# Kernel tuning notes

Measured on AMD Instinct MI355X. Metric: run time of the kernel, lower is better.

## Reference

```python
import jax, jax.numpy as jnp
import numpy as np

# Constants matching init_kwargs
N_HEADS = 8
D_MODEL = 256
PATCH_NUM = 128
D_K = D_MODEL // N_HEADS  # 32
TEMP = 0.5
EPS = 1e-10


def setup_inputs() -> dict:
    key = jax.random.key(0)
    ks = jax.random.split(key, 20)
    s = 0.02
    d, h, n = D_MODEL, N_HEADS, PATCH_NUM
    inp = {
        "x": jax.random.normal(ks[0], (32, n, d), dtype=jnp.float32),
        "gumbel_u": jax.random.uniform(ks[1], (h, n, n, 2), dtype=jnp.float32),
        "memory_w": jax.random.normal(ks[2], (n, h * d), dtype=jnp.float32) * s,
        "fc_out_w": jax.random.normal(ks[3], (2 * d, d), dtype=jnp.float32) * s,
        "fc_out_b": jnp.zeros((d,), jnp.float32),
        "fc_cat_w": jax.random.normal(ks[4], (d, 2), dtype=jnp.float32) * s,
        "fc_cat_b": jnp.zeros((2,), jnp.float32),
        "wq": jax.random.normal(ks[5], (d, d), dtype=jnp.float32) * s,
        "bq": jnp.zeros((d,), jnp.float32),
        "wk": jax.random.normal(ks[6], (d, d), dtype=jnp.float32) * s,
        "bk": jnp.zeros((d,), jnp.float32),
        "wv": jax.random.normal(ks[7], (d, d), dtype=jnp.float32) * s,
        "bv": jnp.zeros((d,), jnp.float32),
        "out_w": jax.random.normal(ks[8], (d, d), dtype=jnp.float32) * s,
        "out_b": jnp.zeros((d,), jnp.float32),
        "mlp_w1": jax.random.normal(ks[9], (d, d), dtype=jnp.float32) * s,
        "mlp_b1": jnp.zeros((d,), jnp.float32),
        "mlp_w2": jax.random.normal(ks[10], (d, d), dtype=jnp.float32) * s,
        "mlp_b2": jnp.zeros((d,), jnp.float32),
    }
    return inp


def _forward(x, memory_w, fc_out_w, fc_out_b, fc_cat_w, fc_cat_b,
             wq, bq, wk, bk, wv, bv, out_w, out_b,
             mlp_w1, mlp_b1, mlp_w2, mlp_b2, gumbel_u):
    H, N, D = N_HEADS, PATCH_NUM, D_MODEL
    B = x.shape[0]

    # ---- SSConnectionLearning on memory feats ----
    # memory: Embedding(N, d_model*n_heads) -> feats [H, N, D]
    feats = memory_w.reshape(N, H, D).transpose(1, 0, 2)
    # rel_rec gathers row index i (receiver), rel_send gathers col index j (sender)
    senders = jnp.broadcast_to(feats[:, None, :, :], (H, N, N, D))   # feats[j]
    receivers = jnp.broadcast_to(feats[:, :, None, :], (H, N, N, D))  # feats[i]
    pair = jnp.concatenate([senders, receivers], axis=-1)  # [H,N,N,2D]
    hdn = jax.nn.relu(jnp.einsum('hijc,cd->hijd', pair, fc_out_w) + fc_out_b)
    logits = jnp.einsum('hijd,dk->hijk', hdn, fc_cat_w) + fc_cat_b  # [H,N,N,2]

    # gumbel-softmax, hard=True, straight-through
    g = -jnp.log(-jnp.log(gumbel_u + EPS) + EPS)
    y_soft = jax.nn.softmax((logits + g) / TEMP, axis=-1)
    y_hard = jax.nn.one_hot(jnp.argmax(y_soft, axis=-1), 2, dtype=y_soft.dtype)
    y = jax.lax.stop_gradient(y_hard - y_soft) + y_soft
    conn = y[..., 1]  # [H,N,N] learned sparse connection mask

    # ---- PatchIntegration (GELU MLP, dropout = identity in eval) ----
    xm = jax.nn.gelu(x @ mlp_w1 + mlp_b1)
    xm = xm @ mlp_w2 + mlp_b2

    # ---- Multihead attention masked by connection matrix ----
    q = (xm @ wq + bq).reshape(B, N, H, D_K).transpose(0, 2, 1, 3)  # [B,H,N,dk]
    k = (xm @ wk + bk).reshape(B, N, H, D_K).transpose(0, 2, 1, 3)
    v = (xm @ wv + bv).reshape(B, N, H, D_K).transpose(0, 2, 1, 3)
    scale = D_K ** -0.5
    scores = jnp.einsum('bhqd,bhkd->bhqk', q, k) * scale
    # additive mask: blocked where conn==0 (large negative keeps softmax finite)
    scores = scores + (conn[None] - 1.0) * 1e9
    attn = jax.nn.softmax(scores, axis=-1)
    out = jnp.einsum('bhqk,bhkd->bhqd', attn, v)
    out = out.transpose(0, 2, 1, 3).reshape(B, N, H * D_K)
    out = out @ out_w + out_b
    return out


def reference(x, gumbel_u, memory_w, fc_out_w, fc_out_b, fc_cat_w, fc_cat_b,
              wq, bq, wk, bk, wv, bv, out_w, out_b,
              mlp_w1, mlp_b1, mlp_w2, mlp_b2):
    return _forward(x, memory_w, fc_out_w, fc_out_b, fc_cat_w, fc_cat_b,
                    wq, bq, wk, bk, wv, bv, out_w, out_b,
                    mlp_w1, mlp_b1, mlp_w2, mlp_b2, gumbel_u)
```

## Files before the change

kernel.cpp:

```cpp
#include <hip/hip_runtime.h>
#include <hip/hip_bf16.h>
#include <math.h>


typedef short short8 __attribute__((ext_vector_type(8)));
typedef float f32x4 __attribute__((ext_vector_type(4)));

union V8 { uint4 u; short8 s; };

__device__ __forceinline__ float gelu_f(float x) {
    float inner = 0.7978845608028654f * (x + 0.044715f * x * x * x);
    return 0.5f * x * (1.0f + tanhf(inner));
}
__device__ __forceinline__ void split_bf16(float x, ushort& h, ushort& l) {
    __hip_bfloat16 bh = __float2bfloat16(x);
    float hf = __bfloat162float(bh);
    __hip_bfloat16 bl = __float2bfloat16(x - hf);
    h = __builtin_bit_cast(ushort, bh);
    l = __builtin_bit_cast(ushort, bl);
}
__device__ __forceinline__ ushort bf16bits(float x) {
    return __builtin_bit_cast(ushort, __float2bfloat16(x));
}
__device__ __forceinline__ float bits_to_f(ushort v) {
    return __builtin_bit_cast(float, ((uint)v) << 16);
}
__device__ __forceinline__ short8 lds_frag(const ushort* p) {
    V8 v; v.u = *(const uint4*)p; return v.s;
}


__global__ __launch_bounds__(512) void k_wprep(
    const float* __restrict__ mlp_w1, const float* __restrict__ mlp_w2,
    const float* __restrict__ wq, const float* __restrict__ wk,
    const float* __restrict__ wv, const float* __restrict__ out_w,
    const float* __restrict__ fc_out_w,
    ushort* __restrict__ hi, ushort* __restrict__ lo) {
    __shared__ __align__(16) float xs2[2][32 * 132];
    int bx = blockIdx.x, t = threadIdx.x;
    int half = t >> 8, tl = t & 255;
    int job = bx * 2 + half;
    int m = job >> 4, ks = (job >> 1) & 7, nh = job & 1;
    const float* W = m == 0 ? mlp_w1 : m == 1 ? mlp_w2 : m == 2 ? wq :
                     m == 3 ? wk : m == 4 ? wv : m == 5 ? out_w :
                     m == 6 ? fc_out_w : fc_out_w + 65536;
    ushort* Hm = hi + m * 65536;
    ushort* Lm = lo + m * 65536;
    float* xs = xs2[half];
    #pragma unroll
    for (int p = 0; p < 4; ++p) {
        int idx = p * 256 + tl;
        int row = idx >> 5, c4 = (idx & 31) * 4;
        *(float4*)(xs + row * 132 + c4) =
            *(const float4*)(W + (ks * 32 + row) * 256 + nh * 128 + c4);
    }
    __syncthreads();
    int lane = tl & 63, lr = lane & 15, quad = lane >> 4;
    #pragma unroll
    for (int it = 0; it < 2; ++it) {
        int tgl = (tl >> 6) + 4 * it;
        int tg = nh * 8 + tgl;
        int nl = tgl * 16 + lr;
        ushort hb[8], lb[8];
        #pragma unroll
        for (int j = 0; j < 8; ++j)
            split_bf16(xs[(quad * 8 + j) * 132 + nl], hb[j], lb[j]);
        uint4 ph = { (uint)hb[0] | ((uint)hb[1] << 16), (uint)hb[2] | ((uint)hb[3] << 16),
                     (uint)hb[4] | ((uint)hb[5] << 16), (uint)hb[6] | ((uint)hb[7] << 16) };
        uint4 pl = { (uint)lb[0] | ((uint)lb[1] << 16), (uint)lb[2] | ((uint)lb[3] << 16),
                     (uint)lb[4] | ((uint)lb[5] << 16), (uint)lb[6] | ((uint)lb[7] << 16) };
        int idx = ((tg * 8 + ks) * 64 + lane) * 8;
        *(uint4*)(Hm + idx) = ph;
        *(uint4*)(Lm + idx) = pl;
    }
}

__global__ __launch_bounds__(512) void k_p2(
    const float* __restrict__ memory_w, const float* __restrict__ X,
    const ushort* __restrict__ Whi, const ushort* __restrict__ Wlo,
    const float* __restrict__ b1, const float* __restrict__ b2,
    const float* __restrict__ Bq, const float* __restrict__ Bk,
    const float* __restrict__ Bv,
    float* __restrict__ A, float* __restrict__ Bm,
    ushort* __restrict__ Q, ushort* __restrict__ K, ushort* __restrict__ V) {
    __shared__ __align__(16) union {
        struct { ushort xhi[16 * 264], xlo[16 * 264]; } f;
        struct {
            ushort aHi[16 * 264], aLo[16 * 264];
            ushort bHi[16 * 264], bLo[16 * 264];
        } g;
    } sm;
    int bx = blockIdx.x, t = threadIdx.x;
    if (bx < 64) {
        int rt = bx;
        #pragma unroll
        for (int ii = 0; ii < 2; ++ii) {
            int f4 = ii * 512 + t;
            int rr = f4 >> 6, c = (f4 & 63) * 4;
            int r = rt * 16 + rr;
            int h = r >> 7, n = r & 127;
            float4 xv = *(const float4*)(memory_w + n * 2048 + h * 256 + c);
            ushort hh[4], ll[4];
            split_bf16(xv.x, hh[0], ll[0]); split_bf16(xv.y, hh[1], ll[1]);
            split_bf16(xv.z, hh[2], ll[2]); split_bf16(xv.w, hh[3], ll[3]);
            uint2 ph = { (uint)hh[0] | ((uint)hh[1] << 16), (uint)hh[2] | ((uint)hh[3] << 16) };
            uint2 pl = { (uint)ll[0] | ((uint)ll[1] << 16), (uint)ll[2] | ((uint)ll[3] << 16) };
            *(uint2*)(sm.f.xhi + rr * 264 + c) = ph;
            *(uint2*)(sm.f.xlo + rr * 264 + c) = pl;
        }
        __syncthreads();
        int lane = t & 63, w = t >> 6;
        int lr = lane & 15, quad = lane >> 4;
        int msel = w & 1, cq = w >> 1;
        const uint4* H4 = (const uint4*)(Whi + (6 + msel) * 65536);
        const uint4* L4 = (const uint4*)(Wlo + (6 + msel) * 65536);
        const ushort* ah = sm.f.xhi + lr * 264 + quad * 8;
        const ushort* al = sm.f.xlo + lr * 264 + quad * 8;
        float* O = msel ? Bm : A;
        #pragma unroll
        for (int i = 0; i < 4; ++i) {
            int tg = cq * 4 + i;
            f32x4 acc = {};
            #pragma unroll
            for (int ks = 0; ks < 8; ++ks) {
                short8 a_h = lds_frag(ah + ks * 32);
                short8 a_l = lds_frag(al + ks * 32);
                int off = (tg * 8 + ks) * 64 + lane;
                V8 bh, bl; bh.u = H4[off]; bl.u = L4[off];
                acc = __builtin_amdgcn_mfma_f32_16x16x32_bf16(a_h, bh.s, acc, 0, 0, 0);
                acc = __builtin_amdgcn_mfma_f32_16x16x32_bf16(a_l, bh.s, acc, 0, 0, 0);
                acc = __builtin_amdgcn_mfma_f32_16x16x32_bf16(a_h, bl.s, acc, 0, 0, 0);
            }
            int n0 = tg * 16 + lr;
            #pragma unroll
            for (int r = 0; r < 4; ++r)
                O[(rt * 16 + quad * 4 + r) * 256 + n0] = acc[r];
        }
        return;
    }
    int r0 = (bx - 64) * 16;
    #pragma unroll
    for (int ii = 0; ii < 2; ++ii) {
        int f4 = ii * 512 + t;
        int row = f4 >> 6, c = (f4 & 63) * 4;
        float4 xv = *(const float4*)(X + (r0 + row) * 256 + c);
        ushort h[4], l[4];
        split_bf16(xv.x, h[0], l[0]); split_bf16(xv.y, h[1], l[1]);
        split_bf16(xv.z, h[2], l[2]); split_bf16(xv.w, h[3], l[3]);
        uint2 ph = { (uint)h[0] | ((uint)h[1] << 16), (uint)h[2] | ((uint)h[3] << 16) };
        uint2 pl = { (uint)l[0] | ((uint)l[1] << 16), (uint)l[2] | ((uint)l[3] << 16) };
        *(uint2*)(sm.g.aHi + row * 264 + c) = ph;
        *(uint2*)(sm.g.aLo + row * 264 + c) = pl;
    }
    __syncthreads();
    int lane = t & 63, w = t >> 6;
    int lr = lane & 15, quad = lane >> 4;
    int aoff = lr * 264 + quad * 8;
    {
        const uint4* H4 = (const uint4*)(Whi + 0 * 65536);
        const uint4* L4 = (const uint4*)(Wlo + 0 * 65536);
        f32x4 acc[2] = {};
        #pragma unroll
        for (int ks = 0; ks < 8; ++ks) {
            short8 a_h = lds_frag(sm.g.aHi + aoff + ks * 32);
            short8 a_l = lds_frag(sm.g.aLo + aoff + ks * 32);
            #pragma unroll
            for (int ti = 0; ti < 2; ++ti) {
                int off = ((w * 2 + ti) * 8 + ks) * 64 + lane;
                V8 bh, bl; bh.u = H4[off]; bl.u = L4[off];
                acc[ti] = __builtin_amdgcn_mfma_f32_16x16x32_bf16(a_h, bh.s, acc[ti], 0, 0, 0);
                acc[ti] = __builtin_amdgcn_mfma_f32_16x16x32_bf16(a_l, bh.s, acc[ti], 0, 0, 0);
                acc[ti] = __builtin_amdgcn_mfma_f32_16x16x32_bf16(a_h, bl.s, acc[ti], 0, 0, 0);
            }
        }
        #pragma unroll
        for (int ti = 0; ti < 2; ++ti) {
            int n0 = (w * 2 + ti) * 16 + lr;
            float bb = b1[n0];
            #pragma unroll
            for (int r = 0; r < 4; ++r) {
                float o = gelu_f(acc[ti][r] + bb);
                ushort hh, ll; split_bf16(o, hh, ll);
                int ad = (quad * 4 + r) * 264 + n0;
                sm.g.bHi[ad] = hh; sm.g.bLo[ad] = ll;
            }
        }
    }
    __syncthreads();
    {
        const uint4* H4 = (const uint4*)(Whi + 1 * 65536);
        const uint4* L4 = (const uint4*)(Wlo + 1 * 65536);
        f32x4 acc[2] = {};
        #pragma unroll
        for (int ks = 0; ks < 8; ++ks) {
            short8 a_h = lds_frag(sm.g.bHi + aoff + ks * 32);
            short8 a_l = lds_frag(sm.g.bLo + aoff + ks * 32);
            #pragma unroll
            for (int ti = 0; ti < 2; ++ti) {
                int off = ((w * 2 + ti) * 8 + ks) * 64 + lane;
                V8 bh, bl; bh.u = H4[off]; bl.u = L4[off];
                acc[ti] = __builtin_amdgcn_mfma_f32_16x16x32_bf16(a_h, bh.s, acc[ti], 0, 0, 0);
                acc[ti] = __builtin_amdgcn_mfma_f32_16x16x32_bf16(a_l, bh.s, acc[ti], 0, 0, 0);
                acc[ti] = __builtin_amdgcn_mfma_f32_16x16x32_bf16(a_h, bl.s, acc[ti], 0, 0, 0);
            }
        }
        __syncthreads();
        #pragma unroll
        for (int ti = 0; ti < 2; ++ti) {
            int n0 = (w * 2 + ti) * 16 + lr;
            float bb = b2[n0];
            #pragma unroll
            for (int r = 0; r < 4; ++r) {
                float o = acc[ti][r] + bb;
                ushort hh, ll; split_bf16(o, hh, ll);
                int ad = (quad * 4 + r) * 264 + n0;
                sm.g.aHi[ad] = hh; sm.g.aLo[ad] = ll;
            }
        }
    }
    __syncthreads();
    {
        const uint4* Hq = (const uint4*)(Whi + 2 * 65536);
        const uint4* Lq = (const uint4*)(Wlo + 2 * 65536);
        const uint4* Hk = (const uint4*)(Whi + 3 * 65536);
        const uint4* Lk = (const uint4*)(Wlo + 3 * 65536);
        const uint4* Hv = (const uint4*)(Whi + 4 * 65536);
        const uint4* Lv = (const uint4*)(Wlo + 4 * 65536);
        f32x4 aq[2] = {}, ak[2] = {}, av[2] = {};
        #pragma unroll 2
        for (int ks = 0; ks < 8; ++ks) {
            short8 a_h = lds_frag(sm.g.aHi + aoff + ks * 32);
            short8 a_l = lds_frag(sm.g.aLo + aoff + ks * 32);
            #pragma unroll
            for (int ti = 0; ti < 2; ++ti) {
                int off = ((w * 2 + ti) * 8 + ks) * 64 + lane;
                V8 qh, ql, kh, kl, vh, vl;
                qh.u = Hq[off]; ql.u = Lq[off];
                kh.u = Hk[off]; kl.u = Lk[off];
                vh.u = Hv[off]; vl.u = Lv[off];
                aq[ti] = __builtin_amdgcn_mfma_f32_16x16x32_bf16(a_h, qh.s, aq[ti], 0, 0, 0);
                aq[ti] = __builtin_amdgcn_mfma_f32_16x16x32_bf16(a_l, qh.s, aq[ti], 0, 0, 0);
                aq[ti] = __builtin_amdgcn_mfma_f32_16x16x32_bf16(a_h, ql.s, aq[ti], 0, 0, 0);
                ak[ti] = __builtin_amdgcn_mfma_f32_16x16x32_bf16(a_h, kh.s, ak[ti], 0, 0, 0);
                ak[ti] = __builtin_amdgcn_mfma_f32_16x16x32_bf16(a_l, kh.s, ak[ti], 0, 0, 0);
                ak[ti] = __builtin_amdgcn_mfma_f32_16x16x32_bf16(a_h, kl.s, ak[ti], 0, 0, 0);
                av[ti] = __builtin_amdgcn_mfma_f32_16x16x32_bf16(a_h, vh.s, av[ti], 0, 0, 0);
                av[ti] = __builtin_amdgcn_mfma_f32_16x16x32_bf16(a_l, vh.s, av[ti], 0, 0, 0);
                av[ti] = __builtin_amdgcn_mfma_f32_16x16x32_bf16(a_h, vl.s, av[ti], 0, 0, 0);
            }
        }
        #pragma unroll
        for (int ti = 0; ti < 2; ++ti) {
            int n0 = (w * 2 + ti) * 16 + lr;
            float bq = Bq[n0], bk = Bk[n0], bv = Bv[n0];
            #pragma unroll
            for (int r = 0; r < 4; ++r) {
                int go = (r0 + quad * 4 + r) * 256 + n0;
                Q[go] = bf16bits(aq[ti][r] + bq);
                K[go] = bf16bits(ak[ti][r] + bk);
                V[go] = bf16bits(av[ti][r] + bv);
            }
        }
    }
}

__global__ __launch_bounds__(512) void k_conn(
    const float* __restrict__ A, const float* __restrict__ Bmat,
    const float* __restrict__ fc_out_b, const float* __restrict__ fc_cat_w,
    const float* __restrict__ fc_cat_b, const float* __restrict__ gumbel_u,
    ushort* __restrict__ maskb) {
    __shared__ __align__(16) float sA[16 * 260], sB[32 * 260];
    int bx = blockIdx.x, t = threadIdx.x;
    int h = bx >> 5;
    int rem = bx & 31;
    int it = rem >> 3, jt = rem & 7;
    int i0 = it * 32, j0 = jt * 16;
    int jl = t & 15, il = t >> 4;
    #pragma unroll
    for (int p = 0; p < 6; ++p) {
        int id2 = p * 512 + t;
        if (id2 < 1024) {
            int rr = id2 >> 6, c = (id2 & 63) * 4;
            *(float4*)(sA + rr * 260 + c) =
                *(const float4*)(A + (h * 128 + j0 + rr) * 256 + c);
        } else {
            int id3 = id2 - 1024;
            int rr = id3 >> 6, c = (id3 & 63) * 4;
            float4 bv = *(const float4*)(Bmat + (h * 128 + i0 + rr) * 256 + c);
            float4 fb = *(const float4*)(fc_out_b + c);
            bv.x += fb.x; bv.y += fb.y; bv.z += fb.z; bv.w += fb.w;
            *(float4*)(sB + rr * 260 + c) = bv;
        }
    }
    __syncthreads();
    const float* Ar = sA + jl * 260;
    const float* Br = sB + il * 260;
    float l0 = fc_cat_b[0], l1 = fc_cat_b[1];
    #pragma unroll 4
    for (int d4 = 0; d4 < 64; ++d4) {
        int d = d4 * 4;
        float4 av = *(const float4*)(Ar + d);
        float4 bv = *(const float4*)(Br + d);
        float4 cwA = *(const float4*)(fc_cat_w + d * 2);
        float4 cwB = *(const float4*)(fc_cat_w + d * 2 + 4);
        float h0 = fmaxf(av.x + bv.x, 0.f);
        float h1 = fmaxf(av.y + bv.y, 0.f);
        float h2 = fmaxf(av.z + bv.z, 0.f);
        float h3 = fmaxf(av.w + bv.w, 0.f);
        l0 += h0 * cwA.x + h1 * cwA.z + h2 * cwB.x + h3 * cwB.z;
        l1 += h0 * cwA.y + h1 * cwA.w + h2 * cwB.y + h3 * cwB.w;
    }
    int i = i0 + il, j = j0 + jl;
    float2 uu = *(const float2*)(gumbel_u + ((h * 128 + i) * 128 + j) * 2);
    float g0 = -logf(-logf(uu.x + 1e-10f) + 1e-10f);
    float g1 = -logf(-logf(uu.y + 1e-10f) + 1e-10f);
    bool on = (l1 + g1) > (l0 + g0);
    maskb[(h * 128 + i) * 128 + j] = bf16bits(on ? 0.f : -1e9f);
}

__global__ __launch_bounds__(256) void k_attn_mfma(
    const ushort* __restrict__ Q, const ushort* __restrict__ K,
    const ushort* __restrict__ V, const ushort* __restrict__ maskb,
    float* __restrict__ AO) {
    int bx = blockIdx.x;
    int b = bx >> 4, h = (bx >> 1) & 7, rh = bx & 1;
    int t = threadIdx.x;
    int lane = t & 63, w = t >> 6;
    __shared__ __align__(16) ushort vT[32 * 136];
    __shared__ __align__(16) ushort ps[64 * 136];
    #pragma unroll
    for (int it = 0; it < 2; ++it) {
        int idx = it * 256 + t;
        int key = idx >> 2, dq8 = (idx & 3) * 8;
        V8 vv; vv.u = *(const uint4*)(V + (b * 128 + key) * 256 + h * 32 + dq8);
        #pragma unroll
        for (int m = 0; m < 8; ++m)
            vT[(dq8 + m) * 136 + key] = (ushort)vv.s[m];
    }
    __syncthreads();
    int lr = lane & 15, quad = lane >> 4;
    int rt = rh * 4 + w;
    V8 af;
    af.u = *(const uint4*)(Q + (b * 128 + rt * 16 + lr) * 256 + h * 32 + quad * 8);
    f32x4 s[8];
    #pragma unroll
    for (int ct = 0; ct < 8; ++ct) {
        V8 bf_;
        bf_.u = *(const uint4*)(K + (b * 128 + ct * 16 + lr) * 256 + h * 32 + quad * 8);
        f32x4 z = {0.f, 0.f, 0.f, 0.f};
        s[ct] = __builtin_amdgcn_mfma_f32_16x16x32_bf16(af.s, bf_.s, z, 0, 0, 0);
    }
    const float scale = 0.17677669529663687f;
    const ushort* mrow = maskb + h * 16384;
    #pragma unroll
    for (int r = 0; r < 4; ++r) {
        int lrow = w * 16 + quad * 4 + r;
        int grow = rt * 16 + quad * 4 + r;
        float sv[8];
        float mx = -3.0e38f;
        #pragma unroll
        for (int ct = 0; ct < 8; ++ct) {
            float bias = bits_to_f(mrow[grow * 128 + ct * 16 + lr]);
            sv[ct] = s[ct][r] * scale + bias;
            mx = fmaxf(mx, sv[ct]);
        }
        mx = fmaxf(mx, __shfl_xor(mx, 1));
        mx = fmaxf(mx, __shfl_xor(mx, 2));
        mx = fmaxf(mx, __shfl_xor(mx, 4));
        mx = fmaxf(mx, __shfl_xor(mx, 8));
        float sum = 0.f;
        #pragma unroll
        for (int ct = 0; ct < 8; ++ct) {
            sv[ct] = __expf(sv[ct] - mx);
            sum += sv[ct];
        }
        sum += __shfl_xor(sum, 1);
        sum += __shfl_xor(sum, 2);
        sum += __shfl_xor(sum, 4);
        sum += __shfl_xor(sum, 8);
        float iv = 1.f / sum;
        #pragma unroll
        for (int ct = 0; ct < 8; ++ct)
            ps[lrow * 136 + ct * 16 + lr] = bf16bits(sv[ct] * iv);
    }
    f32x4 o0 = {}, o1 = {};
    #pragma unroll
    for (int kk = 0; kk < 4; ++kk) {
        short8 pa = lds_frag(ps + (w * 16 + lr) * 136 + kk * 32 + quad * 8);
        short8 v0 = lds_frag(vT + lr * 136 + kk * 32 + quad * 8);
        short8 v1 = lds_frag(vT + (16 + lr) * 136 + kk * 32 + quad * 8);
        o0 = __builtin_amdgcn_mfma_f32_16x16x32_bf16(pa, v0, o0, 0, 0, 0);
        o1 = __builtin_amdgcn_mfma_f32_16x16x32_bf16(pa, v1, o1, 0, 0, 0);
    }
    #pragma unroll
    for (int r = 0; r < 4; ++r) {
        int grow = rt * 16 + quad * 4 + r;
        float* op = AO + b * 32768 + grow * 256 + h * 32;
        op[lr] = o0[r];
        op[16 + lr] = o1[r];
    }
}

__global__ __launch_bounds__(256) void k_gemm16(
    const float* __restrict__ X, const ushort* __restrict__ Whi,
    const ushort* __restrict__ Wlo, const float* __restrict__ bias,
    float* __restrict__ Y) {
    __shared__ __align__(16) ushort xhi[16 * 264], xlo[16 * 264];
    int t = threadIdx.x;
    int r0 = blockIdx.x * 16;
    #pragma unroll
    for (int ii = 0; ii < 4; ++ii) {
        int f4 = ii * 256 + t;
        int row = f4 >> 6, c = (f4 & 63) * 4;
        float4 xv = *(const float4*)(X + (r0 + row) * 256 + c);
        ushort h[4], l[4];
        split_bf16(xv.x, h[0], l[0]); split_bf16(xv.y, h[1], l[1]);
        split_bf16(xv.z, h[2], l[2]); split_bf16(xv.w, h[3], l[3]);
        uint2 ph = { (uint)h[0] | ((uint)h[1] << 16), (uint)h[2] | ((uint)h[3] << 16) };
        uint2 pl = { (uint)l[0] | ((uint)l[1] << 16), (uint)l[2] | ((uint)l[3] << 16) };
        *(uint2*)(xhi + row * 264 + c) = ph;
        *(uint2*)(xlo + row * 264 + c) = pl;
    }
    __syncthreads();
    int l = t & 63, w = t >> 6;
    int lr = l & 15, quad = l >> 4;
    int tg = blockIdx.y * 4 + w;
    const ushort* ah = xhi + lr * 264 + quad * 8;
    const ushort* al = xlo + lr * 264 + quad * 8;
    const uint4* H4 = (const uint4*)Whi;
    const uint4* L4 = (const uint4*)Wlo;
    f32x4 acc = {};
    #pragma unroll
    for (int ks = 0; ks < 8; ++ks) {
        short8 a_h = lds_frag(ah + ks * 32);
        short8 a_l = lds_frag(al + ks * 32);
        int off = (tg * 8 + ks) * 64 + l;
        V8 bh, bl; bh.u = H4[off]; bl.u = L4[off];
        acc = __builtin_amdgcn_mfma_f32_16x16x32_bf16(a_h, bh.s, acc, 0, 0, 0);
        acc = __builtin_amdgcn_mfma_f32_16x16x32_bf16(a_l, bh.s, acc, 0, 0, 0);
        acc = __builtin_amdgcn_mfma_f32_16x16x32_bf16(a_h, bl.s, acc, 0, 0, 0);
    }
    int n0 = tg * 16 + lr;
    float bs = bias[n0];
    #pragma unroll
    for (int r = 0; r < 4; ++r)
        Y[(r0 + quad * 4 + r) * 256 + n0] = acc[r] + bs;
}

extern "C" void kernel_launch(void* const* d_in, const int* in_sizes, int n_in,
                              void* d_out, int out_size, void* d_ws, size_t ws_size,
                              hipStream_t stream) {
    const float* x        = (const float*)d_in[0];
    const float* gumbel_u = (const float*)d_in[1];
    const float* memory_w = (const float*)d_in[2];
    const float* fc_out_w = (const float*)d_in[3];
    const float* fc_out_b = (const float*)d_in[4];
    const float* fc_cat_w = (const float*)d_in[5];
    const float* fc_cat_b = (const float*)d_in[6];
    const float* wq       = (const float*)d_in[7];
    const float* bq       = (const float*)d_in[8];
    const float* wk       = (const float*)d_in[9];
    const float* bk       = (const float*)d_in[10];
    const float* wv_      = (const float*)d_in[11];
    const float* bv_      = (const float*)d_in[12];
    const float* out_w    = (const float*)d_in[13];
    const float* out_b    = (const float*)d_in[14];
    const float* mlp_w1   = (const float*)d_in[15];
    const float* mlp_b1   = (const float*)d_in[16];
    const float* mlp_w2   = (const float*)d_in[17];
    const float* mlp_b2   = (const float*)d_in[18];

    float* ws    = (float*)d_ws;
    float* A     = ws;
    float* Bm    = ws + 262144;
    ushort* mask = (ushort*)(ws + 524288);
    ushort* qb   = (ushort*)(ws + 589824);
    ushort* kb   = (ushort*)(ws + 1114112);
    ushort* vb   = (ushort*)(ws + 1638400);
    float* ao    = ws + 2162688;
    ushort* wf_hi = (ushort*)(ws + 3211264);
    ushort* wf_lo = wf_hi + 8 * 65536;
    float* out   = (float*)d_out;

    k_wprep<<<dim3(64), dim3(512), 0, stream>>>(
        mlp_w1, mlp_w2, wq, wk, wv_, out_w, fc_out_w, wf_hi, wf_lo);
    k_p2<<<dim3(320), dim3(512), 0, stream>>>(
        memory_w, x, wf_hi, wf_lo, mlp_b1, mlp_b2, bq, bk, bv_,
        A, Bm, qb, kb, vb);
    k_conn<<<dim3(256), dim3(512), 0, stream>>>(
        A, Bm, fc_out_b, fc_cat_w, fc_cat_b, gumbel_u, mask);
    k_attn_mfma<<<dim3(512), dim3(256), 0, stream>>>(qb, kb, vb, mask, ao);
    k_gemm16<<<dim3(256, 4), dim3(256), 0, stream>>>(ao, wf_hi + 5 * 65536,
                                                     wf_lo + 5 * 65536, out_b, out);
}
```

Before: 145.2 us.

## Fuse all stages into one cooperative megakernel with grid-wide syncs

Replaces the five separate launches (weight prep, projections, connection mask, attention, output GEMM) with a single cooperative kernel of 256 blocks that separates the phases with grid.sync(). The MLP and QKV projections are chained per row tile through shared memory, and Q/K/V plus the attention output are written in new layouts (V transposed, output split into hi/lo). The aim is to remove launch overhead and inter-kernel gaps. In exchange, every phase must fit one fixed grid size and pay for grid-wide barriers.

```diff
diff --git a/kernel.cpp b/kernel.cpp
--- a/kernel.cpp
+++ b/kernel.cpp
@@ -1,6 +1,9 @@
 #include <hip/hip_runtime.h>
+#include <hip/hip_cooperative_groups.h>
 #include <hip/hip_bf16.h>
 #include <math.h>
+
+namespace cg = cooperative_groups;
 
 
 typedef short short8 __attribute__((ext_vector_type(8)));
@@ -30,37 +33,52 @@
 }
 
 
-__global__ __launch_bounds__(512) void k_wprep(
-    const float* __restrict__ mlp_w1, const float* __restrict__ mlp_w2,
-    const float* __restrict__ wq, const float* __restrict__ wk,
-    const float* __restrict__ wv, const float* __restrict__ out_w,
-    const float* __restrict__ fc_out_w,
-    ushort* __restrict__ hi, ushort* __restrict__ lo) {
-    __shared__ __align__(16) float xs2[2][32 * 132];
+__global__ __launch_bounds__(512) void k_mega(
+    const float* __restrict__ X, const float* __restrict__ gumbel_u,
+    const float* __restrict__ memory_w, const float* __restrict__ fc_out_w,
+    const float* __restrict__ fc_out_b, const float* __restrict__ fc_cat_w,
+    const float* __restrict__ fc_cat_b,
+    const float* __restrict__ wq, const float* __restrict__ Bq,
+    const float* __restrict__ wk, const float* __restrict__ Bk,
+    const float* __restrict__ wv, const float* __restrict__ Bv,
+    const float* __restrict__ out_w, const float* __restrict__ out_b,
+    const float* __restrict__ mlp_w1, const float* __restrict__ b1,
+    const float* __restrict__ mlp_w2, const float* __restrict__ b2,
+    float* __restrict__ A, float* __restrict__ Bm,
+    ushort* __restrict__ maskb,
+    ushort* __restrict__ Qn, ushort* __restrict__ Kn, ushort* __restrict__ Vt,
+    ushort* __restrict__ aoHi, ushort* __restrict__ aoLo,
+    ushort* __restrict__ wf_hi, ushort* __restrict__ wf_lo,
+    float* __restrict__ out) {
+    cg::grid_group grid = cg::this_grid();
+    __shared__ __align__(16) union {
+        struct { float xs[32 * 132]; } w;
+        struct { ushort aHi[16 * 264], aLo[16 * 264],
+                        bHi[16 * 264], bLo[16 * 264]; } g;
+        struct { float sA[16 * 260], sB[32 * 260]; } c;
+        struct { ushort ps[2][64 * 136]; } a;
+    } sm;
     int bx = blockIdx.x, t = threadIdx.x;
-    int half = t >> 8, tl = t & 255;
-    int job = bx * 2 + half;
-    int m = job >> 4, ks = (job >> 1) & 7, nh = job & 1;
-    const float* W = m == 0 ? mlp_w1 : m == 1 ? mlp_w2 : m == 2 ? wq :
-                     m == 3 ? wk : m == 4 ? wv : m == 5 ? out_w :
-                     m == 6 ? fc_out_w : fc_out_w + 65536;
-    ushort* Hm = hi + m * 65536;
-    ushort* Lm = lo + m * 65536;
-    float* xs = xs2[half];
-    #pragma unroll
-    for (int p = 0; p < 4; ++p) {
-        int idx = p * 256 + tl;
-        int row = idx >> 5, c4 = (idx & 31) * 4;
-        *(float4*)(xs + row * 132 + c4) =
-            *(const float4*)(W + (ks * 32 + row) * 256 + nh * 128 + c4);
-    }
-    __syncthreads();
-    int lane = tl & 63, lr = lane & 15, quad = lane >> 4;
-    #pragma unroll
-    for (int it = 0; it < 2; ++it) {
-        int tgl = (tl >> 6) + 4 * it;
-        int tg = nh * 8 + tgl;
-        int nl = tgl * 16 + lr;
+    int lane = t & 63, w = t >> 6, lr = lane & 15, quad = lane >> 4;
+
+    if (bx < 128) {
+        int m = bx >> 4, ks = (bx >> 1) & 7, nh = bx & 1;
+        const float* W = m == 0 ? mlp_w1 : m == 1 ? mlp_w2 : m == 2 ? wq :
+                         m == 3 ? wk : m == 4 ? wv : m == 5 ? out_w :
+                         m == 6 ? fc_out_w : fc_out_w + 65536;
+        ushort* Hm = wf_hi + m * 65536;
+        ushort* Lm = wf_lo + m * 65536;
+        float* xs = sm.w.xs;
+        #pragma unroll
+        for (int p = 0; p < 2; ++p) {
+            int idx = p * 512 + t;
+            int row = idx >> 5, c4 = (idx & 31) * 4;
+            *(float4*)(xs + row * 132 + c4) =
+                *(const float4*)(W + (ks * 32 + row) * 256 + nh * 128 + c4);
+        }
+        __syncthreads();
+        int tg = nh * 8 + w;
+        int nl = w * 16 + lr;
         ushort hb[8], lb[8];
         #pragma unroll
         for (int j = 0; j < 8; ++j)
@@ -73,53 +91,35 @@
         *(uint4*)(Hm + idx) = ph;
         *(uint4*)(Lm + idx) = pl;
     }
-}
-
-__global__ __launch_bounds__(512) void k_p2(
-    const float* __restrict__ memory_w, const float* __restrict__ X,
-    const ushort* __restrict__ Whi, const ushort* __restrict__ Wlo,
-    const float* __restrict__ b1, const float* __restrict__ b2,
-    const float* __restrict__ Bq, const float* __restrict__ Bk,
-    const float* __restrict__ Bv,
-    float* __restrict__ A, float* __restrict__ Bm,
-    ushort* __restrict__ Q, ushort* __restrict__ K, ushort* __restrict__ V) {
-    __shared__ __align__(16) union {
-        struct { ushort xhi[16 * 264], xlo[16 * 264]; } f;
-        struct {
-            ushort aHi[16 * 264], aLo[16 * 264];
-            ushort bHi[16 * 264], bLo[16 * 264];
-        } g;
-    } sm;
-    int bx = blockIdx.x, t = threadIdx.x;
-    if (bx < 64) {
-        int rt = bx;
+    grid.sync();
+
+    if (bx < 128) {
+        int rt = bx >> 1, half = bx & 1;
         #pragma unroll
         for (int ii = 0; ii < 2; ++ii) {
             int f4 = ii * 512 + t;
             int rr = f4 >> 6, c = (f4 & 63) * 4;
             int r = rt * 16 + rr;
-            int h = r >> 7, n = r & 127;
-            float4 xv = *(const float4*)(memory_w + n * 2048 + h * 256 + c);
-            ushort hh[4], ll[4];
-            split_bf16(xv.x, hh[0], ll[0]); split_bf16(xv.y, hh[1], ll[1]);
-            split_bf16(xv.z, hh[2], ll[2]); split_bf16(xv.w, hh[3], ll[3]);
-            uint2 ph = { (uint)hh[0] | ((uint)hh[1] << 16), (uint)hh[2] | ((uint)hh[3] << 16) };
-            uint2 pl = { (uint)ll[0] | ((uint)ll[1] << 16), (uint)ll[2] | ((uint)ll[3] << 16) };
-            *(uint2*)(sm.f.xhi + rr * 264 + c) = ph;
-            *(uint2*)(sm.f.xlo + rr * 264 + c) = pl;
-        }
-        __syncthreads();
-        int lane = t & 63, w = t >> 6;
-        int lr = lane & 15, quad = lane >> 4;
-        int msel = w & 1, cq = w >> 1;
-        const uint4* H4 = (const uint4*)(Whi + (6 + msel) * 65536);
-        const uint4* L4 = (const uint4*)(Wlo + (6 + msel) * 65536);
-        const ushort* ah = sm.f.xhi + lr * 264 + quad * 8;
-        const ushort* al = sm.f.xlo + lr * 264 + quad * 8;
+            int hh = r >> 7, n = r & 127;
+            float4 xv = *(const float4*)(memory_w + n * 2048 + hh * 256 + c);
+            ushort h4[4], l4[4];
+            split_bf16(xv.x, h4[0], l4[0]); split_bf16(xv.y, h4[1], l4[1]);
+            split_bf16(xv.z, h4[2], l4[2]); split_bf16(xv.w, h4[3], l4[3]);
+            uint2 ph = { (uint)h4[0] | ((uint)h4[1] << 16), (uint)h4[2] | ((uint)h4[3] << 16) };
+            uint2 pl = { (uint)l4[0] | ((uint)l4[1] << 16), (uint)l4[2] | ((uint)l4[3] << 16) };
+            *(uint2*)(sm.g.aHi + rr * 264 + c) = ph;
+            *(uint2*)(sm.g.aLo + rr * 264 + c) = pl;
+        }
+        __syncthreads();
+        int msel = w & 1, wp = w >> 1;
+        const uint4* H4 = (const uint4*)(wf_hi + (6 + msel) * 65536);
+        const uint4* L4 = (const uint4*)(wf_lo + (6 + msel) * 65536);
+        const ushort* ah = sm.g.aHi + lr * 264 + quad * 8;
+        const ushort* al = sm.g.aLo + lr * 264 + quad * 8;
         float* O = msel ? Bm : A;
         #pragma unroll
-        for (int i = 0; i < 4; ++i) {
-            int tg = cq * 4 + i;
+        for (int i2 = 0; i2 < 2; ++i2) {
+            int tg = half * 8 + wp * 2 + i2;
             f32x4 acc = {};
             #pragma unroll
             for (int ks = 0; ks < 8; ++ks) {
@@ -136,315 +136,289 @@
             for (int r = 0; r < 4; ++r)
                 O[(rt * 16 + quad * 4 + r) * 256 + n0] = acc[r];
         }
-        return;
-    }
-    int r0 = (bx - 64) * 16;
-    #pragma unroll
-    for (int ii = 0; ii < 2; ++ii) {
-        int f4 = ii * 512 + t;
-        int row = f4 >> 6, c = (f4 & 63) * 4;
-        float4 xv = *(const float4*)(X + (r0 + row) * 256 + c);
-        ushort h[4], l[4];
-        split_bf16(xv.x, h[0], l[0]); split_bf16(xv.y, h[1], l[1]);
-        split_bf16(xv.z, h[2], l[2]); split_bf16(xv.w, h[3], l[3]);
-        uint2 ph = { (uint)h[0] | ((uint)h[1] << 16), (uint)h[2] | ((uint)h[3] << 16) };
-        uint2 pl = { (uint)l[0] | ((uint)l[1] << 16), (uint)l[2] | ((uint)l[3] << 16) };
-        *(uint2*)(sm.g.aHi + row * 264 + c) = ph;
-        *(uint2*)(sm.g.aLo + row * 264 + c) = pl;
-    }
-    __syncthreads();
-    int lane = t & 63, w = t >> 6;
-    int lr = lane & 15, quad = lane >> 4;
-    int aoff = lr * 264 + quad * 8;
+        __syncthreads();
+    }
+
     {
-        const uint4* H4 = (const uint4*)(Whi + 0 * 65536);
-        const uint4* L4 = (const uint4*)(Wlo + 0 * 65536);
+        int r0 = bx * 16;
+        #pragma unroll
+        for (int ii = 0; ii < 2; ++ii) {
+            int f4 = ii * 512 + t;
+            int row = f4 >> 6, c = (f4 & 63) * 4;
+            float4 xv = *(const float4*)(X + (r0 + row) * 256 + c);
+            ushort h4[4], l4[4];
+            split_bf16(xv.x, h4[0], l4[0]); split_bf16(xv.y, h4[1], l4[1]);
+            split_bf16(xv.z, h4[2], l4[2]); split_bf16(xv.w, h4[3], l4[3]);
+            uint2 ph = { (uint)h4[0] | ((uint)h4[1] << 16), (uint)h4[2] | ((uint)h4[3] << 16) };
+            uint2 pl = { (uint)l4[0] | ((uint)l4[1] << 16), (uint)l4[2] | ((uint)l4[3] << 16) };
+            *(uint2*)(sm.g.aHi + row * 264 + c) = ph;
+            *(uint2*)(sm.g.aLo + row * 264 + c) = pl;
+        }
+        __syncthreads();
+        int aoff = lr * 264 + quad * 8;
+        {
+            const uint4* H4 = (const uint4*)(wf_hi + 0 * 65536);
+            const uint4* L4 = (const uint4*)(wf_lo + 0 * 65536);
+            f32x4 acc[2] = {};
+            #pragma unroll
+            for (int ks = 0; ks < 8; ++ks) {
+                short8 a_h = lds_frag(sm.g.aHi + aoff + ks * 32);
+                short8 a_l = lds_frag(sm.g.aLo + aoff + ks * 32);
+                #pragma unroll
+                for (int ti = 0; ti < 2; ++ti) {
+                    int off = ((w * 2 + ti) * 8 + ks) * 64 + lane;
+                    V8 bh, bl; bh.u = H4[off]; bl.u = L4[off];
+                    acc[ti] = __builtin_amdgcn_mfma_f32_16x16x32_bf16(a_h, bh.s, acc[ti], 0, 0, 0);
+                    acc[ti] = __builtin_amdgcn_mfma_f32_16x16x32_bf16(a_l, bh.s, acc[ti], 0, 0, 0);
+                    acc[ti] = __builtin_amdgcn_mfma_f32_16x16x32_bf16(a_h, bl.s, acc[ti], 0, 0, 0);
+                }
+            }
+            #pragma unroll
+            for (int ti = 0; ti < 2; ++ti) {
+                int n0 = (w * 2 + ti) * 16 + lr;
+                float bb = b1[n0];
+                #pragma unroll
+                for (int r = 0; r < 4; ++r) {
+                    float o = gelu_f(acc[ti][r] + bb);
+                    ushort hh, ll; split_bf16(o, hh, ll);
+                    int ad = (quad * 4 + r) * 264 + n0;
+                    sm.g.bHi[ad] = hh; sm.g.bLo[ad] = ll;
+                }
+            }
+        }
+        __syncthreads();
+        {
+            const uint4* H4 = (const uint4*)(wf_hi + 1 * 65536);
+            const uint4* L4 = (const uint4*)(wf_lo + 1 * 65536);
+            f32x4 acc[2] = {};
+            #pragma unroll
+            for (int ks = 0; ks < 8; ++ks) {
+                short8 a_h = lds_frag(sm.g.bHi + aoff + ks * 32);
+                short8 a_l = lds_frag(sm.g.bLo + aoff + ks * 32);
+                #pragma unroll
+                for (int ti = 0; ti < 2; ++ti) {
+                    int off = ((w * 2 + ti) * 8 + ks) * 64 + lane;
+                    V8 bh, bl; bh.u = H4[off]; bl.u = L4[off];
+                    acc[ti] = __builtin_amdgcn_mfma_f32_16x16x32_bf16(a_h, bh.s, acc[ti], 0, 0, 0);
+                    acc[ti] = __builtin_amdgcn_mfma_f32_16x16x32_bf16(a_l, bh.s, acc[ti], 0, 0, 0);
+                    acc[ti] = __builtin_amdgcn_mfma_f32_16x16x32_bf16(a_h, bl.s, acc[ti], 0, 0, 0);
+                }
+            }
+            __syncthreads();
+            #pragma unroll
+            for (int ti = 0; ti < 2; ++ti) {
+                int n0 = (w * 2 + ti) * 16 + lr;
+                float bb = b2[n0];
+                #pragma unroll
+                for (int r = 0; r < 4; ++r) {
+                    float o = acc[ti][r] + bb;
+                    ushort hh, ll; split_bf16(o, hh, ll);
+                    int ad = (quad * 4 + r) * 264 + n0;
+                    sm.g.aHi[ad] = hh; sm.g.aLo[ad] = ll;
+                }
+            }
+        }
+        __syncthreads();
+        {
+            const uint4* Hq = (const uint4*)(wf_hi + 2 * 65536);
+            const uint4* Lq = (const uint4*)(wf_lo + 2 * 65536);
+            const uint4* Hk = (const uint4*)(wf_hi + 3 * 65536);
+            const uint4* Lk = (const uint4*)(wf_lo + 3 * 65536);
+            const uint4* Hv = (const uint4*)(wf_hi + 4 * 65536);
+            const uint4* Lv = (const uint4*)(wf_lo + 4 * 65536);
+            f32x4 aq[2] = {}, ak[2] = {}, av[2] = {};
+            #pragma unroll 2
+            for (int ks = 0; ks < 8; ++ks) {
+                short8 a_h = lds_frag(sm.g.aHi + aoff + ks * 32);
+                short8 a_l = lds_frag(sm.g.aLo + aoff + ks * 32);
+                #pragma unroll
+                for (int ti = 0; ti < 2; ++ti) {
+                    int off = ((w * 2 + ti) * 8 + ks) * 64 + lane;
+                    V8 qh, ql, kh, kl, vh, vl;
+                    qh.u = Hq[off]; ql.u = Lq[off];
+                    kh.u = Hk[off]; kl.u = Lk[off];
+                    vh.u = Hv[off]; vl.u = Lv[off];
+                    aq[ti] = __builtin_amdgcn_mfma_f32_16x16x32_bf16(a_h, qh.s, aq[ti], 0, 0, 0);
+                    aq[ti] = __builtin_amdgcn_mfma_f32_16x16x32_bf16(a_l, qh.s, aq[ti], 0, 0, 0);
+                    aq[ti] = __builtin_amdgcn_mfma_f32_16x16x32_bf16(a_h, ql.s, aq[ti], 0, 0, 0);
+                    ak[ti] = __builtin_amdgcn_mfma_f32_16x16x32_bf16(a_h, kh.s, ak[ti], 0, 0, 0);
+                    ak[ti] = __builtin_amdgcn_mfma_f32_16x16x32_bf16(a_l, kh.s, ak[ti], 0, 0, 0);
+                    ak[ti] = __builtin_amdgcn_mfma_f32_16x16x32_bf16(a_h, kl.s, ak[ti], 0, 0, 0);
+                    av[ti] = __builtin_amdgcn_mfma_f32_16x16x32_bf16(a_h, vh.s, av[ti], 0, 0, 0);
+                    av[ti] = __builtin_amdgcn_mfma_f32_16x16x32_bf16(a_l, vh.s, av[ti], 0, 0, 0);
+                    av[ti] = __builtin_amdgcn_mfma_f32_16x16x32_bf16(a_h, vl.s, av[ti], 0, 0, 0);
+                }
+            }
+            #pragma unroll
+            for (int ti = 0; ti < 2; ++ti) {
+                int n0 = (w * 2 + ti) * 16 + lr;
+                int hh = n0 >> 5, dk = n0 & 31;
+                float vbq = Bq[n0], vbk = Bk[n0], vbv = Bv[n0];
+                #pragma unroll
+                for (int r = 0; r < 4; ++r) {
+                    int row = r0 + quad * 4 + r;
+                    int bb = row >> 7, n = row & 127;
+                    int bh_ = bb * 8 + hh;
+                    Qn[(bh_ * 128 + n) * 32 + dk] = bf16bits(aq[ti][r] + vbq);
+                    Kn[(bh_ * 128 + n) * 32 + dk] = bf16bits(ak[ti][r] + vbk);
+                    Vt[(bh_ * 32 + dk) * 128 + n] = bf16bits(av[ti][r] + vbv);
+                }
+            }
+        }
+    }
+    grid.sync();
+
+    {
+        int h = bx >> 5;
+        int rem = bx & 31;
+        int it = rem >> 3, jt = rem & 7;
+        int i0 = it * 32, j0 = jt * 16;
+        int jl = t & 15, il = t >> 4;
+        #pragma unroll
+        for (int p = 0; p < 6; ++p) {
+            int id2 = p * 512 + t;
+            if (id2 < 1024) {
+                int rr = id2 >> 6, c = (id2 & 63) * 4;
+                *(float4*)(sm.c.sA + rr * 260 + c) =
+                    *(const float4*)(A + (h * 128 + j0 + rr) * 256 + c);
+            } else {
+                int id3 = id2 - 1024;
+                int rr = id3 >> 6, c = (id3 & 63) * 4;
+                float4 bvv = *(const float4*)(Bm + (h * 128 + i0 + rr) * 256 + c);
+                float4 fb = *(const float4*)(fc_out_b + c);
+                bvv.x += fb.x; bvv.y += fb.y; bvv.z += fb.z; bvv.w += fb.w;
+                *(float4*)(sm.c.sB + rr * 260 + c) = bvv;
+            }
+        }
+        __syncthreads();
+        const float* Ar = sm.c.sA + jl * 260;
+        const float* Br = sm.c.sB + il * 260;
+        float l0 = fc_cat_b[0], l1 = fc_cat_b[1];
+        #pragma unroll 4
+        for (int d4 = 0; d4 < 64; ++d4) {
+            int d = d4 * 4;
+            float4 avv = *(const float4*)(Ar + d);
+            float4 bvv = *(const float4*)(Br + d);
+            float4 cwA = *(const float4*)(fc_cat_w + d * 2);
+            float4 cwB = *(const float4*)(fc_cat_w + d * 2 + 4);
+            float h0 = fmaxf(avv.x + bvv.x, 0.f);
+            float h1 = fmaxf(avv.y + bvv.y, 0.f);
+            float h2 = fmaxf(avv.z + bvv.z, 0.f);
+            float h3 = fmaxf(avv.w + bvv.w, 0.f);
+            l0 += h0 * cwA.x + h1 * cwA.z + h2 * cwB.x + h3 * cwB.z;
+            l1 += h0 * cwA.y + h1 * cwA.w + h2 * cwB.y + h3 * cwB.w;
+        }
+        int i = i0 + il, j = j0 + jl;
+        float2 uu = *(const float2*)(gumbel_u + ((h * 128 + i) * 128 + j) * 2);
+        float g0 = -logf(-logf(uu.x + 1e-10f) + 1e-10f);
+        float g1 = -logf(-logf(uu.y + 1e-10f) + 1e-10f);
+        bool on = (l1 + g1) > (l0 + g0);
+        maskb[(h * 128 + i) * 128 + j] = bf16bits(on ? 0.f : -1e9f);
+    }
+    grid.sync();
+
+    {
+        int jh = t >> 8;
+        int job = bx * 2 + jh;
+        int b = job >> 4, h = (job >> 1) & 7, rh = job & 1;
+        int w4 = w & 3;
+        int rt = rh * 4 + w4;
+        int bh_ = b * 8 + h;
+        ushort* ps = sm.a.ps[jh];
+        V8 af;
+        af.u = *(const uint4*)(Qn + (bh_ * 128 + rt * 16 + lr) * 32 + quad * 8);
+        f32x4 s[8];
+        #pragma unroll
+        for (int ct = 0; ct < 8; ++ct) {
+            V8 bf_;
+            bf_.u = *(const uint4*)(Kn + (bh_ * 128 + ct * 16 + lr) * 32 + quad * 8);
+            f32x4 z = {0.f, 0.f, 0.f, 0.f};
+            s[ct] = __builtin_amdgcn_mfma_f32_16x16x32_bf16(af.s, bf_.s, z, 0, 0, 0);
+        }
+        const float scale = 0.17677669529663687f;
+        const ushort* mrow = maskb + h * 16384;
+        #pragma unroll
+        for (int r = 0; r < 4; ++r) {
+            int lrow = w4 * 16 + quad * 4 + r;
+            int grow = rt * 16 + quad * 4 + r;
+            float sv[8];
+            float mx = -3.0e38f;
+            #pragma unroll
+            for (int ct = 0; ct < 8; ++ct) {
+                float bias = bits_to_f(mrow[grow * 128 + ct * 16 + lr]);
+                sv[ct] = s[ct][r] * scale + bias;
+                mx = fmaxf(mx, sv[ct]);
+            }
+            mx = fmaxf(mx, __shfl_xor(mx, 1));
+            mx = fmaxf(mx, __shfl_xor(mx, 2));
+            mx = fmaxf(mx, __shfl_xor(mx, 4));
+            mx = fmaxf(mx, __shfl_xor(mx, 8));
+            float sum = 0.f;
+            #pragma unroll
+            for (int ct = 0; ct < 8; ++ct) {
+                sv[ct] = __expf(sv[ct] - mx);
+                sum += sv[ct];
+            }
+            sum += __shfl_xor(sum, 1);
+            sum += __shfl_xor(sum, 2);
+            sum += __shfl_xor(sum, 4);
+            sum += __shfl_xor(sum, 8);
+            float iv = 1.f / sum;
+            #pragma unroll
+            for (int ct = 0; ct < 8; ++ct)
+                ps[lrow * 136 + ct * 16 + lr] = bf16bits(sv[ct] * iv);
+        }
+        f32x4 o0 = {}, o1 = {};
+        #pragma unroll
+        for (int kk = 0; kk < 4; ++kk) {
+            short8 pa = lds_frag(ps + (w4 * 16 + lr) * 136 + kk * 32 + quad * 8);
+            V8 v0, v1;
+            v0.u = *(const uint4*)(Vt + (bh_ * 32 + lr) * 128 + kk * 32 + quad * 8);
+            v1.u = *(const uint4*)(Vt + (bh_ * 32 + 16 + lr) * 128 + kk * 32 + quad * 8);
+            o0 = __builtin_amdgcn_mfma_f32_16x16x32_bf16(pa, v0.s, o0, 0, 0, 0);
+            o1 = __builtin_amdgcn_mfma_f32_16x16x32_bf16(pa, v1.s, o1, 0, 0, 0);
+        }
+        #pragma unroll
+        for (int r = 0; r < 4; ++r) {
+            int grow = rt * 16 + quad * 4 + r;
+            int base = (b * 128 + grow) * 256 + h * 32;
+            ushort hh, ll;
+            split_bf16(o0[r], hh, ll);
+            aoHi[base + lr] = hh; aoLo[base + lr] = ll;
+            split_bf16(o1[r], hh, ll);
+            aoHi[base + 16 + lr] = hh; aoLo[base + 16 + lr] = ll;
+        }
+    }
+    grid.sync();
+
+    {
+        int r0 = bx * 16;
+        const uint4* H4 = (const uint4*)(wf_hi + 5 * 65536);
+        const uint4* L4 = (const uint4*)(wf_lo + 5 * 65536);
         f32x4 acc[2] = {};
         #pragma unroll
         for (int ks = 0; ks < 8; ++ks) {
-            short8 a_h = lds_frag(sm.g.aHi + aoff + ks * 32);
-            short8 a_l = lds_frag(sm.g.aLo + aoff + ks * 32);
+            V8 ahv, alv;
+            ahv.u = *(const uint4*)(aoHi + (r0 + lr) * 256 + ks * 32 + quad * 8);
+            alv.u = *(const uint4*)(aoLo + (r0 + lr) * 256 + ks * 32 + quad * 8);
             #pragma unroll
             for (int ti = 0; ti < 2; ++ti) {
                 int off = ((w * 2 + ti) * 8 + ks) * 64 + lane;
                 V8 bh, bl; bh.u = H4[off]; bl.u = L4[off];
-                acc[ti] = __builtin_amdgcn_mfma_f32_16x16x32_bf16(a_h, bh.s, acc[ti], 0, 0, 0);
-                acc[ti] = __builtin_amdgcn_mfma_f32_16x16x32_bf16(a_l, bh.s, acc[ti], 0, 0, 0);
-                acc[ti] = __builtin_amdgcn_mfma_f32_16x16x32_bf16(a_h, bl.s, acc[ti], 0, 0, 0);
+                acc[ti] = __builtin_amdgcn_mfma_f32_16x16x32_bf16(ahv.s, bh.s, acc[ti], 0, 0, 0);
+                acc[ti] = __builtin_amdgcn_mfma_f32_16x16x32_bf16(alv.s, bh.s, acc[ti], 0, 0, 0);
+                acc[ti] = __builtin_amdgcn_mfma_f32_16x16x32_bf16(ahv.s, bl.s, acc[ti], 0, 0, 0);
             }
         }
         #pragma unroll
         for (int ti = 0; ti < 2; ++ti) {
             int n0 = (w * 2 + ti) * 16 + lr;
-            float bb = b1[n0];
-            #pragma unroll
-            for (int r = 0; r < 4; ++r) {
-                float o = gelu_f(acc[ti][r] + bb);
-                ushort hh, ll; split_bf16(o, hh, ll);
-                int ad = (quad * 4 + r) * 264 + n0;
-                sm.g.bHi[ad] = hh; sm.g.bLo[ad] = ll;
-            }
-        }
-    }
-    __syncthreads();
-    {
-        const uint4* H4 = (const uint4*)(Whi + 1 * 65536);
-        const uint4* L4 = (const uint4*)(Wlo + 1 * 65536);
-        f32x4 acc[2] = {};
-        #pragma unroll
-        for (int ks = 0; ks < 8; ++ks) {
-            short8 a_h = lds_frag(sm.g.bHi + aoff + ks * 32);
-            short8 a_l = lds_frag(sm.g.bLo + aoff + ks * 32);
-            #pragma unroll
-            for (int ti = 0; ti < 2; ++ti) {
-                int off = ((w * 2 + ti) * 8 + ks) * 64 + lane;
-                V8 bh, bl; bh.u = H4[off]; bl.u = L4[off];
-                acc[ti] = __builtin_amdgcn_mfma_f32_16x16x32_bf16(a_h, bh.s, acc[ti], 0, 0, 0);
-                acc[ti] = __builtin_amdgcn_mfma_f32_16x16x32_bf16(a_l, bh.s, acc[ti], 0, 0, 0);
-                acc[ti] = __builtin_amdgcn_mfma_f32_16x16x32_bf16(a_h, bl.s, acc[ti], 0, 0, 0);
-            }
-        }
-        __syncthreads();
-        #pragma unroll
-        for (int ti = 0; ti < 2; ++ti) {
-            int n0 = (w * 2 + ti) * 16 + lr;
-            float bb = b2[n0];
-            #pragma unroll
-            for (int r = 0; r < 4; ++r) {
-                float o = acc[ti][r] + bb;
-                ushort hh, ll; split_bf16(o, hh, ll);
-                int ad = (quad * 4 + r) * 264 + n0;
-                sm.g.aHi[ad] = hh; sm.g.aLo[ad] = ll;
-            }
-        }
-    }
-    __syncthreads();
-    {
-        const uint4* Hq = (const uint4*)(Whi + 2 * 65536);
-        const uint4* Lq = (const uint4*)(Wlo + 2 * 65536);
-        const uint4* Hk = (const uint4*)(Whi + 3 * 65536);
-        const uint4* Lk = (const uint4*)(Wlo + 3 * 65536);
-        const uint4* Hv = (const uint4*)(Whi + 4 * 65536);
-        const uint4* Lv = (const uint4*)(Wlo + 4 * 65536);
-        f32x4 aq[2] = {}, ak[2] = {}, av[2] = {};
-        #pragma unroll 2
-        for (int ks = 0; ks < 8; ++ks) {
-            short8 a_h = lds_frag(sm.g.aHi + aoff + ks * 32);
-            short8 a_l = lds_frag(sm.g.aLo + aoff + ks * 32);
-            #pragma unroll
-            for (int ti = 0; ti < 2; ++ti) {
-                int off = ((w * 2 + ti) * 8 + ks) * 64 + lane;
-                V8 qh, ql, kh, kl, vh, vl;
-                qh.u = Hq[off]; ql.u = Lq[off];
-                kh.u = Hk[off]; kl.u = Lk[off];
-                vh.u = Hv[off]; vl.u = Lv[off];
-                aq[ti] = __builtin_amdgcn_mfma_f32_16x16x32_bf16(a_h, qh.s, aq[ti], 0, 0, 0);
-                aq[ti] = __builtin_amdgcn_mfma_f32_16x16x32_bf16(a_l, qh.s, aq[ti], 0, 0, 0);
-                aq[ti] = __builtin_amdgcn_mfma_f32_16x16x32_bf16(a_h, ql.s, aq[ti], 0, 0, 0);
-                ak[ti] = __builtin_amdgcn_mfma_f32_16x16x32_bf16(a_h, kh.s, ak[ti], 0, 0, 0);
-                ak[ti] = __builtin_amdgcn_mfma_f32_16x16x32_bf16(a_l, kh.s, ak[ti], 0, 0, 0);
-                ak[ti] = __builtin_amdgcn_mfma_f32_16x16x32_bf16(a_h, kl.s, ak[ti], 0, 0, 0);
-                av[ti] = __builtin_amdgcn_mfma_f32_16x16x32_bf16(a_h, vh.s, av[ti], 0, 0, 0);
-                av[ti] = __builtin_amdgcn_mfma_f32_16x16x32_bf16(a_l, vh.s, av[ti], 0, 0, 0);
-                av[ti] = __builtin_amdgcn_mfma_f32_16x16x32_bf16(a_h, vl.s, av[ti], 0, 0, 0);
-            }
-        }
-        #pragma unroll
-        for (int ti = 0; ti < 2; ++ti) {
-            int n0 = (w * 2 + ti) * 16 + lr;
-            float bq = Bq[n0], bk = Bk[n0], bv = Bv[n0];
-            #pragma unroll
-            for (int r = 0; r < 4; ++r) {
-                int go = (r0 + quad * 4 + r) * 256 + n0;
-                Q[go] = bf16bits(aq[ti][r] + bq);
-                K[go] = bf16bits(ak[ti][r] + bk);
-                V[go] = bf16bits(av[ti][r] + bv);
-            }
-        }
-    }
-}
-
-__global__ __launch_bounds__(512) void k_conn(
-    const float* __restrict__ A, const float* __restrict__ Bmat,
-    const float* __restrict__ fc_out_b, const float* __restrict__ fc_cat_w,
-    const float* __restrict__ fc_cat_b, const float* __restrict__ gumbel_u,
-    ushort* __restrict__ maskb) {
-    __shared__ __align__(16) float sA[16 * 260], sB[32 * 260];
-    int bx = blockIdx.x, t = threadIdx.x;
-    int h = bx >> 5;
-    int rem = bx & 31;
-    int it = rem >> 3, jt = rem & 7;
-    int i0 = it * 32, j0 = jt * 16;
-    int jl = t & 15, il = t >> 4;
-    #pragma unroll
-    for (int p = 0; p < 6; ++p) {
-        int id2 = p * 512 + t;
-        if (id2 < 1024) {
-            int rr = id2 >> 6, c = (id2 & 63) * 4;
-            *(float4*)(sA + rr * 260 + c) =
-                *(const float4*)(A + (h * 128 + j0 + rr) * 256 + c);
-        } else {
-            int id3 = id2 - 1024;
-            int rr = id3 >> 6, c = (id3 & 63) * 4;
-            float4 bv = *(const float4*)(Bmat + (h * 128 + i0 + rr) * 256 + c);
-            float4 fb = *(const float4*)(fc_out_b + c);
-            bv.x += fb.x; bv.y += fb.y; bv.z += fb.z; bv.w += fb.w;
-            *(float4*)(sB + rr * 260 + c) = bv;
-        }
-    }
-    __syncthreads();
-    const float* Ar = sA + jl * 260;
-    const float* Br = sB + il * 260;
-    float l0 = fc_cat_b[0], l1 = fc_cat_b[1];
-    #pragma unroll 4
-    for (int d4 = 0; d4 < 64; ++d4) {
-        int d = d4 * 4;
-        float4 av = *(const float4*)(Ar + d);
-        float4 bv = *(const float4*)(Br + d);
-        float4 cwA = *(const float4*)(fc_cat_w + d * 2);
-        float4 cwB = *(const float4*)(fc_cat_w + d * 2 + 4);
-        float h0 = fmaxf(av.x + bv.x, 0.f);
-        float h1 = fmaxf(av.y + bv.y, 0.f);
-        float h2 = fmaxf(av.z + bv.z, 0.f);
-        float h3 = fmaxf(av.w + bv.w, 0.f);
-        l0 += h0 * cwA.x + h1 * cwA.z + h2 * cwB.x + h3 * cwB.z;
-        l1 += h0 * cwA.y + h1 * cwA.w + h2 * cwB.y + h3 * cwB.w;
-    }
-    int i = i0 + il, j = j0 + jl;
-    float2 uu = *(const float2*)(gumbel_u + ((h * 128 + i) * 128 + j) * 2);
-    float g0 = -logf(-logf(uu.x + 1e-10f) + 1e-10f);
-    float g1 = -logf(-logf(uu.y + 1e-10f) + 1e-10f);
-    bool on = (l1 + g1) > (l0 + g0);
-    maskb[(h * 128 + i) * 128 + j] = bf16bits(on ? 0.f : -1e9f);
-}
-
-__global__ __launch_bounds__(256) void k_attn_mfma(
-    const ushort* __restrict__ Q, const ushort* __restrict__ K,
-    const ushort* __restrict__ V, const ushort* __restrict__ maskb,
-    float* __restrict__ AO) {
-    int bx = blockIdx.x;
-    int b = bx >> 4, h = (bx >> 1) & 7, rh = bx & 1;
-    int t = threadIdx.x;
-    int lane = t & 63, w = t >> 6;
-    __shared__ __align__(16) ushort vT[32 * 136];
-    __shared__ __align__(16) ushort ps[64 * 136];
-    #pragma unroll
-    for (int it = 0; it < 2; ++it) {
-        int idx = it * 256 + t;
-        int key = idx >> 2, dq8 = (idx & 3) * 8;
-        V8 vv; vv.u = *(const uint4*)(V + (b * 128 + key) * 256 + h * 32 + dq8);
-        #pragma unroll
-        for (int m = 0; m < 8; ++m)
-            vT[(dq8 + m) * 136 + key] = (ushort)vv.s[m];
-    }
-    __syncthreads();
-    int lr = lane & 15, quad = lane >> 4;
-    int rt = rh * 4 + w;
-    V8 af;
-    af.u = *(const uint4*)(Q + (b * 128 + rt * 16 + lr) * 256 + h * 32 + quad * 8);
-    f32x4 s[8];
-    #pragma unroll
-    for (int ct = 0; ct < 8; ++ct) {
-        V8 bf_;
-        bf_.u = *(const uint4*)(K + (b * 128 + ct * 16 + lr) * 256 + h * 32 + quad * 8);
-        f32x4 z = {0.f, 0.f, 0.f, 0.f};
-        s[ct] = __builtin_amdgcn_mfma_f32_16x16x32_bf16(af.s, bf_.s, z, 0, 0, 0);
-    }
-    const float scale = 0.17677669529663687f;
-    const ushort* mrow = maskb + h * 16384;
-    #pragma unroll
-    for (int r = 0; r < 4; ++r) {
-        int lrow = w * 16 + quad * 4 + r;
-        int grow = rt * 16 + quad * 4 + r;
-        float sv[8];
-        float mx = -3.0e38f;
-        #pragma unroll
-        for (int ct = 0; ct < 8; ++ct) {
-            float bias = bits_to_f(mrow[grow * 128 + ct * 16 + lr]);
-            sv[ct] = s[ct][r] * scale + bias;
-            mx = fmaxf(mx, sv[ct]);
-        }
-        mx = fmaxf(mx, __shfl_xor(mx, 1));
-        mx = fmaxf(mx, __shfl_xor(mx, 2));
-        mx = fmaxf(mx, __shfl_xor(mx, 4));
-        mx = fmaxf(mx, __shfl_xor(mx, 8));
-        float sum = 0.f;
-        #pragma unroll
-        for (int ct = 0; ct < 8; ++ct) {
-            sv[ct] = __expf(sv[ct] - mx);
-            sum += sv[ct];
-        }
-        sum += __shfl_xor(sum, 1);
-        sum += __shfl_xor(sum, 2);
-        sum += __shfl_xor(sum, 4);
-        sum += __shfl_xor(sum, 8);
-        float iv = 1.f / sum;
-        #pragma unroll
-        for (int ct = 0; ct < 8; ++ct)
-            ps[lrow * 136 + ct * 16 + lr] = bf16bits(sv[ct] * iv);
-    }
-    f32x4 o0 = {}, o1 = {};
-    #pragma unroll
-    for (int kk = 0; kk < 4; ++kk) {
-        short8 pa = lds_frag(ps + (w * 16 + lr) * 136 + kk * 32 + quad * 8);
-        short8 v0 = lds_frag(vT + lr * 136 + kk * 32 + quad * 8);
-        short8 v1 = lds_frag(vT + (16 + lr) * 136 + kk * 32 + quad * 8);
-        o0 = __builtin_amdgcn_mfma_f32_16x16x32_bf16(pa, v0, o0, 0, 0, 0);
-        o1 = __builtin_amdgcn_mfma_f32_16x16x32_bf16(pa, v1, o1, 0, 0, 0);
-    }
-    #pragma unroll
-    for (int r = 0; r < 4; ++r) {
-        int grow = rt * 16 + quad * 4 + r;
-        float* op = AO + b * 32768 + grow * 256 + h * 32;
-        op[lr] = o0[r];
-        op[16 + lr] = o1[r];
-    }
-}
-
-__global__ __launch_bounds__(256) void k_gemm16(
-    const float* __restrict__ X, const ushort* __restrict__ Whi,
-    const ushort* __restrict__ Wlo, const float* __restrict__ bias,
-    float* __restrict__ Y) {
-    __shared__ __align__(16) ushort xhi[16 * 264], xlo[16 * 264];
-    int t = threadIdx.x;
-    int r0 = blockIdx.x * 16;
-    #pragma unroll
-    for (int ii = 0; ii < 4; ++ii) {
-        int f4 = ii * 256 + t;
-        int row = f4 >> 6, c = (f4 & 63) * 4;
-        float4 xv = *(const float4*)(X + (r0 + row) * 256 + c);
-        ushort h[4], l[4];
-        split_bf16(xv.x, h[0], l[0]); split_bf16(xv.y, h[1], l[1]);
-        split_bf16(xv.z, h[2], l[2]); split_bf16(xv.w, h[3], l[3]);
-        uint2 ph = { (uint)h[0] | ((uint)h[1] << 16), (uint)h[2] | ((uint)h[3] << 16) };
-        uint2 pl = { (uint)l[0] | ((uint)l[1] << 16), (uint)l[2] | ((uint)l[3] << 16) };
-        *(uint2*)(xhi + row * 264 + c) = ph;
-        *(uint2*)(xlo + row * 264 + c) = pl;
-    }
-    __syncthreads();
-    int l = t & 63, w = t >> 6;
-    int lr = l & 15, quad = l >> 4;
-    int tg = blockIdx.y * 4 + w;
-    const ushort* ah = xhi + lr * 264 + quad * 8;
-    const ushort* al = xlo + lr * 264 + quad * 8;
-    const uint4* H4 = (const uint4*)Whi;
-    const uint4* L4 = (const uint4*)Wlo;
-    f32x4 acc = {};
-    #pragma unroll
-    for (int ks = 0; ks < 8; ++ks) {
-        short8 a_h = lds_frag(ah + ks * 32);
-        short8 a_l = lds_frag(al + ks * 32);
-        int off = (tg * 8 + ks) * 64 + l;
-        V8 bh, bl; bh.u = H4[off]; bl.u = L4[off];
-        acc = __builtin_amdgcn_mfma_f32_16x16x32_bf16(a_h, bh.s, acc, 0, 0, 0);
-        acc = __builtin_amdgcn_mfma_f32_16x16x32_bf16(a_l, bh.s, acc, 0, 0, 0);
-        acc = __builtin_amdgcn_mfma_f32_16x16x32_bf16(a_h, bl.s, acc, 0, 0, 0);
-    }
-    int n0 = tg * 16 + lr;
-    float bs = bias[n0];
-    #pragma unroll
-    for (int r = 0; r < 4; ++r)
-        Y[(r0 + quad * 4 + r) * 256 + n0] = acc[r] + bs;
+            float bs = out_b[n0];
+            #pragma unroll
+            for (int r = 0; r < 4; ++r)
+                out[(r0 + quad * 4 + r) * 256 + n0] = acc[ti][r] + bs;
+        }
+    }
 }
 
 extern "C" void kernel_launch(void* const* d_in, const int* in_sizes, int n_in,
@@ -470,26 +444,27 @@
     const float* mlp_w2   = (const float*)d_in[17];
     const float* mlp_b2   = (const float*)d_in[18];
 
-    float* ws    = (float*)d_ws;
-    float* A     = ws;
-    float* Bm    = ws + 262144;
-    ushort* mask = (ushort*)(ws + 524288);
-    ushort* qb   = (ushort*)(ws + 589824);
-    ushort* kb   = (ushort*)(ws + 1114112);
-    ushort* vb   = (ushort*)(ws + 1638400);
-    float* ao    = ws + 2162688;
+    float* ws     = (float*)d_ws;
+    float* A      = ws;
+    float* Bm     = ws + 262144;
+    ushort* mask  = (ushort*)(ws + 524288);
+    ushort* qn    = (ushort*)(ws + 589824);
+    ushort* kn    = (ushort*)(ws + 1114112);
+    ushort* vt    = (ushort*)(ws + 1638400);
+    ushort* aoHi  = (ushort*)(ws + 2162688);
+    ushort* aoLo  = (ushort*)(ws + 2686976);
     ushort* wf_hi = (ushort*)(ws + 3211264);
     ushort* wf_lo = wf_hi + 8 * 65536;
-    float* out   = (float*)d_out;
-
-    k_wprep<<<dim3(64), dim3(512), 0, stream>>>(
-        mlp_w1, mlp_w2, wq, wk, wv_, out_w, fc_out_w, wf_hi, wf_lo);
-    k_p2<<<dim3(320), dim3(512), 0, stream>>>(
-        memory_w, x, wf_hi, wf_lo, mlp_b1, mlp_b2, bq, bk, bv_,
-        A, Bm, qb, kb, vb);
-    k_conn<<<dim3(256), dim3(512), 0, stream>>>(
-        A, Bm, fc_out_b, fc_cat_w, fc_cat_b, gumbel_u, mask);
-    k_attn_mfma<<<dim3(512), dim3(256), 0, stream>>>(qb, kb, vb, mask, ao);
-    k_gemm16<<<dim3(256, 4), dim3(256), 0, stream>>>(ao, wf_hi + 5 * 65536,
-                                                     wf_lo + 5 * 65536, out_b, out);
-}
+    float* out    = (float*)d_out;
+
+    void* args[] = {
+        (void*)&x, (void*)&gumbel_u, (void*)&memory_w, (void*)&fc_out_w,
+        (void*)&fc_out_b, (void*)&fc_cat_w, (void*)&fc_cat_b,
+        (void*)&wq, (void*)&bq, (void*)&wk, (void*)&bk,
+        (void*)&wv_, (void*)&bv_, (void*)&out_w, (void*)&out_b,
+        (void*)&mlp_w1, (void*)&mlp_b1, (void*)&mlp_w2, (void*)&mlp_b2,
+        (void*)&A, (void*)&Bm, (void*)&mask, (void*)&qn, (void*)&kn, (void*)&vt,
+        (void*)&aoHi, (void*)&aoLo, (void*)&wf_hi, (void*)&wf_lo, (void*)&out };
+    hipLaunchCooperativeKernel((const void*)k_mega, dim3(256), dim3(512),
+                               args, 0, stream);
+}
```

Measured after the change: 295.8 us. 104% more time.
